# Kernel optimization log

Measured on AMD Instinct MI355X. Metric: run time of the kernel, lower is better.

Reference implementation:

```python
import jax, jax.numpy as jnp
import numpy as np

B, T, U, V = 8, 128, 64, 512  # batch, enc frames, label length, vocab
U1 = U + 1
BLANK = 0


def setup_inputs() -> dict:
    key = jax.random.key(0)
    k1, k2, k3, k4, k5 = jax.random.split(key, 5)
    trans_acts = jax.random.normal(k1, (B, T, V), jnp.float32)
    pred_acts = jax.random.normal(k2, (B, U1, V), jnp.float32)
    labels = jax.random.randint(k3, (B, U), 1, V).astype(jnp.int32)  # 0 is blank
    act_lens = jax.random.randint(k4, (B,), T // 2, T + 1).astype(jnp.int32)
    label_lens = jax.random.randint(k5, (B,), U // 2, U + 1).astype(jnp.int32)
    return dict(trans_acts=trans_acts, pred_acts=pred_acts, labels=labels,
                act_lens=act_lens, label_lens=label_lens)


def _rnnt_costs(trans_acts, pred_acts, labels, act_lens, label_lens, blank=BLANK):
    # joint log-probs: log_softmax(trans[t] + pred[u]) over vocab -> (B,T,U1,V)
    logits = trans_acts[:, :, None, :] + pred_acts[:, None, :, :]
    logp = jax.nn.log_softmax(logits, axis=-1)
    lp_blank = logp[..., blank]                                    # (B,T,U1)
    # label emission log-prob at (t,u): prob of labels[b,u]        # (B,T,U)
    lp_lab = jnp.take_along_axis(
        logp[:, :, :U, :], labels[:, None, :, None].astype(jnp.int32), axis=-1)[..., 0]

    nb, nu1 = trans_acts.shape[0], pred_acts.shape[1]
    # alpha at t=0: alpha[0,u] = sum_{u'<u} lp_lab[0,u']
    alpha0 = jnp.concatenate(
        [jnp.zeros((nb, 1), logp.dtype), jnp.cumsum(lp_lab[:, 0, :], axis=-1)], axis=1)

    def t_step(alpha_prev, xs):
        blank_prev, lab_cur = xs                 # (B,U1), (B,U)
        a_in = alpha_prev + blank_prev           # vertical (blank) transition

        def u_step(carry, x):
            a, d = x                             # a:(B,) from blank path, d:(B,) label lp
            new = jnp.logaddexp(a, carry + d)
            return new, new

        _, rest = jax.lax.scan(u_step, a_in[:, 0], (a_in[:, 1:].T, lab_cur.T))
        alpha_t = jnp.concatenate([a_in[:, :1], rest.T], axis=1)
        return alpha_t, alpha_t

    xs = (jnp.swapaxes(lp_blank[:, :-1, :], 0, 1),   # blank lp at t-1: (T-1,B,U1)
          jnp.swapaxes(lp_lab[:, 1:, :], 0, 1))      # label lp at t:  (T-1,B,U)
    _, alphas = jax.lax.scan(t_step, alpha0, xs)     # (T-1,B,U1)
    alphas = jnp.concatenate([alpha0[None], alphas], axis=0)  # (T,B,U1)

    b_idx = jnp.arange(nb)
    t_idx = act_lens - 1
    u_idx = label_lens
    ll = alphas[t_idx, b_idx, u_idx] + lp_blank[b_idx, t_idx, u_idx]
    return -ll                                       # per-example cost (B,)


def reference(trans_acts, pred_acts, labels, act_lens, label_lens):
    costs = _rnnt_costs(trans_acts, pred_acts, labels, act_lens, label_lens)
    # size_average=False: return summed cost as a length-1 vector (as torch FloatTensor([sum]))
    return jnp.sum(costs)[None]
```

## Files before the change

### kernel.cpp

```cpp
#include <hip/hip_runtime.h>
#include <math.h>

#define Bn 8
#define Tn 128
#define Un 64
#define U1n 65
#define Vn 512
#define NEG (-1e30f)
#define LOG2E 1.4426950408889634f
#define LN2 0.6931471805599453f

template <int CTRL>
__device__ __forceinline__ float dpp_mv(float x) {
  return __int_as_float(__builtin_amdgcn_update_dpp(
      __float_as_int(x), __float_as_int(x), CTRL, 0xF, 0xF, false));
}

__device__ __forceinline__ float red_sum64(float m) {
  m += dpp_mv<0xB1>(m);
  m += dpp_mv<0x4E>(m);
  m += dpp_mv<0x141>(m);
  m += dpp_mv<0x140>(m);
  m += __shfl_xor(m, 16);
  m += __shfl_xor(m, 32);
  return m;
}

__device__ __forceinline__ float wave_shr1(float x, float fill) {
  return __int_as_float(__builtin_amdgcn_update_dpp(
      __float_as_int(fill), __float_as_int(x), 0x138, 0xF, 0xF, false));
}

__device__ __forceinline__ float hw_exp2(float x) {
  return __builtin_amdgcn_exp2f(x);
}
__device__ __forceinline__ float hw_log2(float x) {
  return __builtin_amdgcn_logf(x);
}

__device__ __forceinline__ float laddexp2(float a, float b) {
  float mx = fmaxf(a, b), mn = fminf(a, b);
  return mx + hw_log2(1.f + hw_exp2(mn - mx));
}

__global__ __launch_bounds__(256) void rnnt_logprobs(
    const float* __restrict__ trans, const float* __restrict__ pred,
    const int* __restrict__ labels, float* __restrict__ lbT,
    float* __restrict__ llT, float* __restrict__ out) {
  if (blockIdx.x == 0 && threadIdx.x == 0) out[0] = 0.f;

  int wave = blockIdx.x * 4 + (threadIdx.x >> 6);
  int lane = threadIdx.x & 63;
  int u = wave % U1n;
  int th = (wave / U1n) & 63;
  int b = wave / (U1n * 64);
  int t0 = th, t1 = th + 64;

  const float* tr0 = trans + (size_t)(b * Tn + t0) * Vn;
  const float* tr1 = trans + (size_t)(b * Tn + t1) * Vn;
  const float* pr = pred + (size_t)(b * U1n + u) * Vn;
  const float4* tr04 = (const float4*)tr0;
  const float4* tr14 = (const float4*)tr1;
  const float4* pr4 = (const float4*)pr;

  float4 pA = pr4[lane], pB = pr4[lane + 64];
  float4 xA = tr04[lane], xB = tr04[lane + 64];
  float4 yA = tr14[lane], yB = tr14[lane + 64];

  float sum0 = __expf(xA.x + pA.x) + __expf(xA.y + pA.y) +
               __expf(xA.z + pA.z) + __expf(xA.w + pA.w) +
               __expf(xB.x + pB.x) + __expf(xB.y + pB.y) +
               __expf(xB.z + pB.z) + __expf(xB.w + pB.w);
  float sum1 = __expf(yA.x + pA.x) + __expf(yA.y + pA.y) +
               __expf(yA.z + pA.z) + __expf(yA.w + pA.w) +
               __expf(yB.x + pB.x) + __expf(yB.y + pB.y) +
               __expf(yB.z + pB.z) + __expf(yB.w + pB.w);
  sum0 = red_sum64(sum0);
  sum1 = red_sum64(sum1);

  if (lane == 0) {
    float lse0 = __logf(sum0);
    float lse1 = __logf(sum1);
    lbT[((size_t)b * U1n + u) * Tn + t0] = (tr0[0] + pr[0] - lse0) * LOG2E;
    lbT[((size_t)b * U1n + u) * Tn + t1] = (tr1[0] + pr[0] - lse1) * LOG2E;
    if (u < Un) {
      int lbl = labels[b * Un + u];
      llT[((size_t)b * Un + u) * Tn + t0] = (tr0[lbl] + pr[lbl] - lse0) * LOG2E;
      llT[((size_t)b * Un + u) * Tn + t1] = (tr1[lbl] + pr[lbl] - lse1) * LOG2E;
    }
  }
}

__global__ __launch_bounds__(64) void rnnt_alpha(
    const float* __restrict__ lbT, const float* __restrict__ llT,
    const int* __restrict__ act_lens, const int* __restrict__ label_lens,
    float* __restrict__ out) {
  int b = blockIdx.x;
  int l = threadIdx.x;

  const float* LBrow = lbT + ((size_t)b * U1n + l + 1) * Tn;
  const float* LLrow = llT + ((size_t)b * Un + l) * Tn;
  const float* L0row = lbT + (size_t)b * U1n * Tn;

  int ti = act_lens[b] - 1;
  int ui = label_lens[b];
  bool is_l0 = (l == 0);
  bool is_rec = (l == ui - 1);

  float a = NEG, p = 0.f, rec = 0.f;
  float lbB[8], llB[8], l0B[8];
#pragma unroll
  for (int k = 0; k < 8; ++k) {
    lbB[k] = LBrow[k - l - 1];
    llB[k] = LLrow[k - l];
    l0B[k] = L0row[k];
  }

  for (int sb = 0; sb < 192; sb += 8) {
#pragma unroll
    for (int k = 0; k < 8; ++k) {
      int s = sb + k;
      float lb_t = lbB[k], ll_t = llB[k], l0_t = l0B[k];
      lbB[k] = LBrow[s + 8 - l - 1];
      llB[k] = LLrow[s + 8 - l];
      l0B[k] = L0row[s + 8];

      float nb = wave_shr1(a, 0.f);
      nb = is_l0 ? p : nb;
      float vert = a + lb_t;
      float horiz = nb + ll_t;
      float an = laddexp2(vert, horiz);
      int t = s - l;
      bool active = (t >= 0);
      a = active ? an : NEG;
      p += l0_t;
      if (active & is_rec & (t == ti)) rec = an;
    }
  }

  float r = __shfl(rec, ui - 1);
  if (l == 0) {
    float lbv = lbT[((size_t)b * U1n + ui) * Tn + ti];
    atomicAdd(out, -(r + lbv) * LN2);
  }
}

extern "C" void kernel_launch(void* const* d_in, const int* in_sizes, int n_in,
                              void* d_out, int out_size, void* d_ws, size_t ws_size,
                              hipStream_t stream) {
  const float* trans = (const float*)d_in[0];
  const float* pred = (const float*)d_in[1];
  const int* labels = (const int*)d_in[2];
  const int* act_lens = (const int*)d_in[3];
  const int* label_lens = (const int*)d_in[4];
  float* out = (float*)d_out;

  float* lbT = (float*)d_ws;
  float* llT = lbT + 66560 + 256;

  int nwaves = Bn * 64 * U1n;
  rnnt_logprobs<<<nwaves / 4, 256, 0, stream>>>(trans, pred, labels, lbT, llT,
                                                out);
  rnnt_alpha<<<Bn, 64, 0, stream>>>(lbT, llT, act_lens, label_lens, out);
}
```

Measured before the change: 29.38 us.

## Factor joint softmax into exp dot products and stop alpha scan at target

The joint normaliser sum_v exp(t+p) is rewritten as a dot product of exp(trans) and exp(pred). Each block caches exp(pred) for one batch element in LDS and computes 4 time frames against all 65 label positions, replacing the per-(t,u) recomputation of 512 exponentials. The alpha recursion loop now stops after the last anti-diagonal it needs (act_len+label_len) instead of always running 192 steps. Lane 0's horizontal input now comes from the DPP shift fill value. The trade-offs: dropping max subtraction risks overflow for large activations, and about 142KB of LDS limits each CU to one block with only 256 blocks in total.

```diff
diff --git a/kernel.cpp b/kernel.cpp
--- a/kernel.cpp
+++ b/kernel.cpp
@@ -9,6 +9,7 @@
 #define NEG (-1e30f)
 #define LOG2E 1.4426950408889634f
 #define LN2 0.6931471805599453f
+#define VP 516
 
 template <int CTRL>
 __device__ __forceinline__ float dpp_mv(float x) {
@@ -26,7 +27,7 @@
   return m;
 }
 
-__device__ __forceinline__ float wave_shr1(float x, float fill) {
+__device__ __forceinline__ float wave_shr1_fill(float x, float fill) {
   return __int_as_float(__builtin_amdgcn_update_dpp(
       __float_as_int(fill), __float_as_int(x), 0x138, 0xF, 0xF, false));
 }
@@ -43,51 +44,97 @@
   return mx + hw_log2(1.f + hw_exp2(mn - mx));
 }
 
-__global__ __launch_bounds__(256) void rnnt_logprobs(
+__global__ __launch_bounds__(256) void rnnt_dots(
     const float* __restrict__ trans, const float* __restrict__ pred,
     const int* __restrict__ labels, float* __restrict__ lbT,
     float* __restrict__ llT, float* __restrict__ out) {
+  __shared__ float EPs[U1n * VP];
+  __shared__ float ETs[4 * VP];
+  __shared__ float pr0s[U1n];
+  __shared__ float prls[Un];
+  __shared__ int lbls[Un];
+
   if (blockIdx.x == 0 && threadIdx.x == 0) out[0] = 0.f;
 
-  int wave = blockIdx.x * 4 + (threadIdx.x >> 6);
-  int lane = threadIdx.x & 63;
-  int u = wave % U1n;
-  int th = (wave / U1n) & 63;
-  int b = wave / (U1n * 64);
-  int t0 = th, t1 = th + 64;
-
-  const float* tr0 = trans + (size_t)(b * Tn + t0) * Vn;
-  const float* tr1 = trans + (size_t)(b * Tn + t1) * Vn;
-  const float* pr = pred + (size_t)(b * U1n + u) * Vn;
-  const float4* tr04 = (const float4*)tr0;
-  const float4* tr14 = (const float4*)tr1;
-  const float4* pr4 = (const float4*)pr;
-
-  float4 pA = pr4[lane], pB = pr4[lane + 64];
-  float4 xA = tr04[lane], xB = tr04[lane + 64];
-  float4 yA = tr14[lane], yB = tr14[lane + 64];
-
-  float sum0 = __expf(xA.x + pA.x) + __expf(xA.y + pA.y) +
-               __expf(xA.z + pA.z) + __expf(xA.w + pA.w) +
-               __expf(xB.x + pB.x) + __expf(xB.y + pB.y) +
-               __expf(xB.z + pB.z) + __expf(xB.w + pB.w);
-  float sum1 = __expf(yA.x + pA.x) + __expf(yA.y + pA.y) +
-               __expf(yA.z + pA.z) + __expf(yA.w + pA.w) +
-               __expf(yB.x + pB.x) + __expf(yB.y + pB.y) +
-               __expf(yB.z + pB.z) + __expf(yB.w + pB.w);
-  sum0 = red_sum64(sum0);
-  sum1 = red_sum64(sum1);
-
+  int b = blockIdx.x >> 5;
+  int chunk = blockIdx.x & 31;
+  int tid = threadIdx.x;
+  int w = tid >> 6;
+  int lane = tid & 63;
+  int t = chunk * 4 + w;
+
+  if (tid < U1n) {
+    pr0s[tid] = pred[((size_t)b * U1n + tid) * Vn];
+    if (tid < Un) {
+      int lbl = labels[b * Un + tid];
+      lbls[tid] = lbl;
+      prls[tid] = pred[((size_t)b * U1n + tid) * Vn + lbl];
+    }
+  }
+
+  const float4* pred4 = (const float4*)(pred + (size_t)b * U1n * Vn);
+#pragma unroll
+  for (int k = 0; k < 33; ++k) {
+    int idx = tid + k * 256;
+    if (idx < U1n * 128) {
+      int u = idx >> 7, j = idx & 127;
+      float4 pv = pred4[u * 128 + j];
+      float4 ev;
+      ev.x = hw_exp2(pv.x * LOG2E);
+      ev.y = hw_exp2(pv.y * LOG2E);
+      ev.z = hw_exp2(pv.z * LOG2E);
+      ev.w = hw_exp2(pv.w * LOG2E);
+      *(float4*)&EPs[u * VP + j * 4] = ev;
+    }
+  }
+
+  const float* trow = trans + ((size_t)b * Tn + t) * Vn;
+  const float4* trow4 = (const float4*)trow;
+  {
+    float4 x0 = trow4[lane], x1 = trow4[lane + 64];
+    float4 e0, e1;
+    e0.x = hw_exp2(x0.x * LOG2E); e0.y = hw_exp2(x0.y * LOG2E);
+    e0.z = hw_exp2(x0.z * LOG2E); e0.w = hw_exp2(x0.w * LOG2E);
+    e1.x = hw_exp2(x1.x * LOG2E); e1.y = hw_exp2(x1.y * LOG2E);
+    e1.z = hw_exp2(x1.z * LOG2E); e1.w = hw_exp2(x1.w * LOG2E);
+    *(float4*)&ETs[w * VP + lane * 8] = e0;
+    *(float4*)&ETs[w * VP + lane * 8 + 4] = e1;
+  }
+  __syncthreads();
+
+  int u = lane;
+  float ac0 = 0.f, ac1 = 0.f, ac2 = 0.f, ac3 = 0.f;
+  int epb = u * VP, etb = w * VP;
+#pragma unroll 4
+  for (int vc = 0; vc < Vn; vc += 4) {
+    float4 ep = *(const float4*)&EPs[epb + vc];
+    float4 et = *(const float4*)&ETs[etb + vc];
+    ac0 += et.x * ep.x;
+    ac1 += et.y * ep.y;
+    ac2 += et.z * ep.z;
+    ac3 += et.w * ep.w;
+  }
+  float dot = (ac0 + ac2) + (ac1 + ac3);
+
+  float p64;
+  {
+    float4 eA = *(const float4*)&EPs[64 * VP + lane * 8];
+    float4 eB = *(const float4*)&EPs[64 * VP + lane * 8 + 4];
+    float4 tA = *(const float4*)&ETs[etb + lane * 8];
+    float4 tB = *(const float4*)&ETs[etb + lane * 8 + 4];
+    float part = eA.x * tA.x + eA.y * tA.y + eA.z * tA.z + eA.w * tA.w +
+                 eB.x * tB.x + eB.y * tB.y + eB.z * tB.z + eB.w * tB.w;
+    p64 = red_sum64(part);
+  }
+
+  float tr0v = trow[0];
+  float lse2 = hw_log2(dot);
+  lbT[((size_t)b * U1n + u) * Tn + t] = (tr0v + pr0s[u]) * LOG2E - lse2;
+  float trl = trow[lbls[u]];
+  llT[((size_t)b * Un + u) * Tn + t] = (trl + prls[u]) * LOG2E - lse2;
   if (lane == 0) {
-    float lse0 = __logf(sum0);
-    float lse1 = __logf(sum1);
-    lbT[((size_t)b * U1n + u) * Tn + t0] = (tr0[0] + pr[0] - lse0) * LOG2E;
-    lbT[((size_t)b * U1n + u) * Tn + t1] = (tr1[0] + pr[0] - lse1) * LOG2E;
-    if (u < Un) {
-      int lbl = labels[b * Un + u];
-      llT[((size_t)b * Un + u) * Tn + t0] = (tr0[lbl] + pr[lbl] - lse0) * LOG2E;
-      llT[((size_t)b * Un + u) * Tn + t1] = (tr1[lbl] + pr[lbl] - lse1) * LOG2E;
-    }
+    lbT[((size_t)b * U1n + 64) * Tn + t] =
+        (tr0v + pr0s[64]) * LOG2E - hw_log2(p64);
   }
 }
 
@@ -104,7 +151,7 @@
 
   int ti = act_lens[b] - 1;
   int ui = label_lens[b];
-  bool is_l0 = (l == 0);
+  int s_end = ti + ui;
   bool is_rec = (l == ui - 1);
 
   float a = NEG, p = 0.f, rec = 0.f;
@@ -116,7 +163,7 @@
     l0B[k] = L0row[k];
   }
 
-  for (int sb = 0; sb < 192; sb += 8) {
+  for (int sb = 0; sb < s_end; sb += 8) {
 #pragma unroll
     for (int k = 0; k < 8; ++k) {
       int s = sb + k;
@@ -125,16 +172,14 @@
       llB[k] = LLrow[s + 8 - l];
       l0B[k] = L0row[s + 8];
 
-      float nb = wave_shr1(a, 0.f);
-      nb = is_l0 ? p : nb;
+      float nb = wave_shr1_fill(a, p);
       float vert = a + lb_t;
       float horiz = nb + ll_t;
       float an = laddexp2(vert, horiz);
       int t = s - l;
-      bool active = (t >= 0);
-      a = active ? an : NEG;
+      a = (t >= 0) ? an : NEG;
       p += l0_t;
-      if (active & is_rec & (t == ti)) rec = an;
+      if ((t == ti) & is_rec) rec = an;
     }
   }
 
@@ -155,11 +200,9 @@
   const int* label_lens = (const int*)d_in[4];
   float* out = (float*)d_out;
 
-  float* lbT = (float*)d_ws;
-  float* llT = lbT + 66560 + 256;
-
-  int nwaves = Bn * 64 * U1n;
-  rnnt_logprobs<<<nwaves / 4, 256, 0, stream>>>(trans, pred, labels, lbT, llT,
-                                                out);
+  float* lbT = (float*)d_ws + 64;
+  float* llT = lbT + Bn * U1n * Tn;
+
+  rnnt_dots<<<Bn * 32, 256, 0, stream>>>(trans, pred, labels, lbT, llT, out);
   rnnt_alpha<<<Bn, 64, 0, stream>>>(lbT, llT, act_lens, label_lens, out);
 }
```

Result: faster. 26.05 us, median of 2 (-11.3%).
